# Optimization experiments

Hardware: AMD Instinct MI355X
Metric: run time of the kernel (lower is better)

Reference implementation:

```python
import jax, jax.numpy as jnp
import numpy as np
import math

H = 128      # hidden_size
B = 4        # bsz
N = 32       # bsz * num_doc_per_q
L = 128      # doc_len


def setup_inputs() -> dict:
    key = jax.random.key(0)
    ks = jax.random.split(key, 7)
    word_ent_info = jax.random.normal(ks[0], (N, L, H), dtype=jnp.float32)
    word_ent_info_mask = jax.random.randint(ks[1], (N, L), 0, 2, dtype=jnp.int32)
    doc = jax.random.normal(ks[2], (N, L, H), dtype=jnp.float32)
    doc_mask = jax.random.randint(ks[3], (N, L), 0, 2, dtype=jnp.int32)
    q_for_text = jax.random.normal(ks[4], (B, H), dtype=jnp.float32)
    # nn.Linear(3H, H): weight [H, 3H], bias [H]
    W1 = jax.random.normal(ks[5], (H, 3 * H), dtype=jnp.float32) / math.sqrt(3 * H)
    b1 = jnp.zeros((H,), dtype=jnp.float32)
    # nn.Linear(H, 1): weight [1, H], bias [1]
    w2 = jax.random.normal(ks[6], (1, H), dtype=jnp.float32) / math.sqrt(H)
    b2 = jnp.zeros((1,), dtype=jnp.float32)
    return {"word_ent_info": word_ent_info, "word_ent_info_mask": word_ent_info_mask,
            "doc": doc, "doc_mask": doc_mask, "q_for_text": q_for_text,
            "W1": W1, "b1": b1, "w2": w2, "b2": b2}


def reference(word_ent_info, word_ent_info_mask, doc, doc_mask, q_for_text, W1, b1, w2, b2):
    n, l, h = doc.shape
    bsz = q_for_text.shape[0]
    dt = doc.dtype

    # word_ent_infoagg = mask^T @ word_ent_info -> [N, H]
    m = word_ent_info_mask.astype(dt)
    ent_agg = jnp.einsum('nl,nlh->nh', m, word_ent_info)

    # q expanded to one row per document: [N, H]
    q_exp = jnp.repeat(q_for_text, n // bsz, axis=0)

    # Split W1 over the concat([doc_self, ent_agg, q_agg]) feature axis.
    # score_pre[n,j,k,:] = W1a @ (doc_j*doc_k) + W1b @ (doc_j*ent_agg) + W1c @ (doc_k*q)
    W1a, W1b, W1c = jnp.split(W1, 3, axis=1)        # each [H, H]
    A = jnp.einsum('nje,nke,ge->njkg', doc, doc, W1a)          # [N,L,L,H]
    Bt = jnp.einsum('nje,ge->njg', doc * ent_agg[:, None, :], W1b)  # [N,L,H]
    Ct = jnp.einsum('nke,ge->nkg', doc * q_exp[:, None, :], W1c)    # [N,L,H]
    hid = jnp.tanh(A + Bt[:, :, None, :] + Ct[:, None, :, :] + b1)  # [N,L,L,H]

    score = (jnp.einsum('njkg,g->njk', hid, w2[0]) + b2[0]) / math.sqrt(h)

    dm = doc_mask.astype(dt)
    score_mask = dm[:, :, None] * dm[:, None, :]     # [N,L,L]
    score = jnp.where(score_mask == 0.0, jnp.asarray(-1e9, dt), score)
    w = jax.nn.softmax(score, axis=-1) * score_mask
    doc_ent_enc = jnp.einsum('njk,nkh->njh', w, doc)  # [N,L,H]
    return doc_ent_enc
```

## Files before the change

### kernel.cpp

```cpp
#include <hip/hip_runtime.h>
#include <hip/hip_bf16.h>
#include <math.h>

#define Hh 128
#define Nn 32
#define Ll 128
#define W1S 384
#define PAD 136
#define EP 64
#define SP 72

typedef __attribute__((ext_vector_type(8))) short short8;
typedef __attribute__((ext_vector_type(4))) float floatx4;
typedef __attribute__((ext_vector_type(8))) _Float16 f16x8;

__device__ __forceinline__ unsigned short f2bf(float x) {
  __hip_bfloat16 h = __float2bfloat16(x);
  return __builtin_bit_cast(unsigned short, h);
}
__device__ __forceinline__ short8 pack8(float4 a, float4 b) {
  short8 r;
  r[0] = (short)f2bf(a.x); r[1] = (short)f2bf(a.y);
  r[2] = (short)f2bf(a.z); r[3] = (short)f2bf(a.w);
  r[4] = (short)f2bf(b.x); r[5] = (short)f2bf(b.y);
  r[6] = (short)f2bf(b.z); r[7] = (short)f2bf(b.w);
  return r;
}
__device__ __forceinline__ f16x8 cvt8h(float4 a, float4 b) {
  f16x8 r;
  r[0] = (_Float16)a.x; r[1] = (_Float16)a.y;
  r[2] = (_Float16)a.z; r[3] = (_Float16)a.w;
  r[4] = (_Float16)b.x; r[5] = (_Float16)b.y;
  r[6] = (_Float16)b.z; r[7] = (_Float16)b.w;
  return r;
}

__launch_bounds__(256, 2)
__global__ void k_prep(const float* __restrict__ wei, const int* __restrict__ wmask,
                       const float* __restrict__ doc, const float* __restrict__ q,
                       const float* __restrict__ W1, const float* __restrict__ b1,
                       float* __restrict__ Bt, float* __restrict__ Ct) {
  __shared__ __align__(16) short Wsb[Hh * PAD];
  __shared__ __align__(16) short docb[64 * PAD];
  __shared__ __align__(16) float red[2][Hh];
  __shared__ __align__(16) float scale[Hh];

  int b = blockIdx.x;
  int n = b >> 2, which = (b >> 1) & 1, mh = b & 1;
  int tid = threadIdx.x;
  const float* docn = doc + (size_t)n * Ll * Hh;
  int e8 = (tid & 15) * 8;

  float4 dreg[4][2];
#pragma unroll
  for (int p = 0; p < 4; ++p) {
    int row = mh * 64 + p * 16 + (tid >> 4);
    const float4* dp = (const float4*)(docn + (size_t)row * Hh + e8);
    dreg[p][0] = dp[0]; dreg[p][1] = dp[1];
  }
#pragma unroll
  for (int p = 0; p < 8; ++p) {
    int row = p * 16 + (tid >> 4);
    const float4* wp = (const float4*)(W1 + (size_t)row * W1S + (which + 1) * Hh + e8);
    *(short8*)(Wsb + row * PAD + e8) = pack8(wp[0], wp[1]);
  }
  if (which == 1) {
    if (tid < Hh) scale[tid] = q[(n >> 3) * Hh + tid];
  } else {
    int e = tid & 127, halfl = tid >> 7;
    const float* wp = wei + (size_t)n * Ll * Hh + (size_t)halfl * 64 * Hh + e;
    const int* mp = wmask + n * Ll + halfl * 64;
    float a = 0.f;
#pragma unroll 16
    for (int l = 0; l < 64; ++l) a = fmaf((float)mp[l], wp[(size_t)l * Hh], a);
    red[halfl][e] = a;
  }
  __syncthreads();
  if (which == 0 && tid < Hh) scale[tid] = red[0][tid] + red[1][tid];
  __syncthreads();
  {
    float s[8];
#pragma unroll
    for (int i = 0; i < 8; ++i) s[i] = scale[e8 + i];
#pragma unroll
    for (int p = 0; p < 4; ++p) {
      int r = p * 16 + (tid >> 4);
      float4 a = dreg[p][0], bq = dreg[p][1];
      a.x *= s[0]; a.y *= s[1]; a.z *= s[2]; a.w *= s[3];
      bq.x *= s[4]; bq.y *= s[5]; bq.z *= s[6]; bq.w *= s[7];
      *(short8*)(docb + r * PAD + e8) = pack8(a, bq);
    }
  }
  __syncthreads();

  int lane = tid & 63, w = tid >> 6;
  int l15 = lane & 15, quad = lane >> 4;
  floatx4 acc[8];
#pragma unroll
  for (int nt = 0; nt < 8; ++nt) acc[nt] = (floatx4){0.f, 0.f, 0.f, 0.f};
#pragma unroll
  for (int c = 0; c < 4; ++c) {
    int eo = c * 32 + quad * 8;
    short8 af = *(const short8*)(docb + (w * 16 + l15) * PAD + eo);
    short8 bfr[8];
#pragma unroll
    for (int nt = 0; nt < 8; ++nt)
      bfr[nt] = *(const short8*)(Wsb + (nt * 16 + l15) * PAD + eo);
#pragma unroll
    for (int nt = 0; nt < 8; ++nt)
      acc[nt] = __builtin_amdgcn_mfma_f32_16x16x32_bf16(af, bfr[nt], acc[nt], 0, 0, 0);
  }

  float* outp = (which ? Ct : Bt) + (size_t)n * Ll * Hh;
#pragma unroll
  for (int nt = 0; nt < 8; ++nt) {
    int g = nt * 16 + l15;
    float badd = which ? 0.f : b1[g];
#pragma unroll
    for (int r = 0; r < 4; ++r) {
      int k = mh * 64 + w * 16 + quad * 4 + r;
      outp[(size_t)k * Hh + g] = acc[nt][r] + badd;
    }
  }
}

__launch_bounds__(512, 6)
__global__ void k_main(const float* __restrict__ doc, const int* __restrict__ dmask,
                       const float* __restrict__ W1,
                       const float* __restrict__ w2, const float* __restrict__ b2,
                       const float* __restrict__ Bt, const float* __restrict__ Ct,
                       float* __restrict__ out) {
  __shared__ __align__(16) _Float16 As[Hh * SP];
  __shared__ __align__(16) _Float16 Bs[Hh * SP];
  __shared__ __align__(16) float sc[Ll];
  __shared__ __align__(16) float scw[Ll];

  int bid = blockIdx.x;
  int n = bid & 31, j = bid >> 5;
  int tid = threadIdx.x;
  const float* docn = doc + (size_t)n * Ll * Hh;
  size_t orow = ((size_t)n * Ll + j) * Hh;

  if (dmask[n * Ll + j] == 0) {
    if (tid < Hh) out[orow + tid] = 0.f;
    return;
  }

  int lane = tid & 63, wv = tid >> 6;
  int l15 = lane & 15, quad = lane >> 4;
  int grow = tid >> 2, seg = (tid & 3) * 16;

  floatx4 acc[8];
#pragma unroll
  for (int nt = 0; nt < 8; ++nt) acc[nt] = (floatx4){0.f, 0.f, 0.f, 0.f};

#pragma unroll
  for (int p = 0; p < 2; ++p) {
    if (p) __syncthreads();
    {
      const float4* dsrc = (const float4*)(docn + (size_t)grow * Hh + p * EP + seg);
      const float4* wsrc = (const float4*)(W1 + (size_t)grow * W1S + p * EP + seg);
      float4 d0 = dsrc[0], d1 = dsrc[1], d2 = dsrc[2], d3 = dsrc[3];
      float4 w0 = wsrc[0], w1 = wsrc[1], w2v = wsrc[2], w3 = wsrc[3];
      *(f16x8*)(Bs + grow * SP + seg) = cvt8h(d0, d1);
      *(f16x8*)(Bs + grow * SP + seg + 8) = cvt8h(d2, d3);
      *(f16x8*)(As + grow * SP + seg) = cvt8h(w0, w1);
      *(f16x8*)(As + grow * SP + seg + 8) = cvt8h(w2v, w3);
    }
    __syncthreads();
#pragma unroll
    for (int c = 0; c < 2; ++c) {
      int eo = c * 32 + quad * 8;
      f16x8 dr = *(const f16x8*)(Bs + (wv * 16 + l15) * SP + eo);
      f16x8 jr = *(const f16x8*)(Bs + j * SP + eo);
      f16x8 af = dr * jr;
#pragma unroll
      for (int nt = 0; nt < 8; ++nt) {
        f16x8 bfr = *(const f16x8*)(As + (nt * 16 + l15) * SP + eo);
        acc[nt] = __builtin_amdgcn_mfma_f32_16x16x32_f16(af, bfr, acc[nt], 0, 0, 0);
      }
    }
  }

  const float c2 = 2.885390081777927f;
  float bbc[8], w2r[8];
  const float* btrow = Bt + orow;
#pragma unroll
  for (int nt = 0; nt < 8; ++nt) {
    int g = nt * 16 + l15;
    bbc[nt] = btrow[g] * c2;
    w2r[nt] = w2[g];
  }
  const float* ctn = Ct + (size_t)n * Ll * Hh;
#pragma unroll
  for (int r = 0; r < 4; ++r) {
    int k = wv * 16 + quad * 4 + r;
    const float* ctp = ctn + (size_t)k * Hh + l15;
    float p = 0.f;
#pragma unroll
    for (int nt = 0; nt < 8; ++nt) {
      float s = acc[nt][r] + ctp[nt * 16];
      float a2 = fmaf(s, c2, bbc[nt]);
      float e = exp2f(a2);
      float th = fmaf(-2.f, __builtin_amdgcn_rcpf(e + 1.f), 1.f);
      p = fmaf(th, w2r[nt], p);
    }
    p += __shfl_xor(p, 1);
    p += __shfl_xor(p, 2);
    p += __shfl_xor(p, 4);
    p += __shfl_xor(p, 8);
    if (l15 == 0) sc[k] = p;
  }
  __syncthreads();

  {
    float b2v = b2[0];
    const float inv = 0.088388347648318447f;
    const int* dmn = dmask + n * Ll;
    int m0 = dmn[lane], m1 = dmn[lane + 64];
    float s0 = (sc[lane] + b2v) * inv;
    float s1 = (sc[lane + 64] + b2v) * inv;
    s0 = m0 ? s0 : -1e9f;
    s1 = m1 ? s1 : -1e9f;
    float mx = fmaxf(s0, s1);
#pragma unroll
    for (int off = 32; off; off >>= 1) mx = fmaxf(mx, __shfl_xor(mx, off));
    float ex0 = __expf(s0 - mx), ex1 = __expf(s1 - mx);
    float sm = ex0 + ex1;
#pragma unroll
    for (int off = 32; off; off >>= 1) sm += __shfl_xor(sm, off);
    float rden = 1.f / sm;
    scw[lane] = m0 ? ex0 * rden : 0.f;
    scw[lane + 64] = m1 ? ex1 * rden : 0.f;
  }
  __syncthreads();

  float* ored = (float*)As;
  int qk = tid >> 7, h = tid & 127;
  const float* dbase = docn + (size_t)qk * 32 * Hh + h;
  float o = 0.f;
#pragma unroll 8
  for (int kk = 0; kk < 32; ++kk)
    o = fmaf(scw[qk * 32 + kk], dbase[(size_t)kk * Hh], o);
  ored[qk * Hh + h] = o;
  __syncthreads();
  if (tid < Ll)
    out[orow + tid] = ored[tid] + ored[Hh + tid] + ored[2 * Hh + tid] + ored[3 * Hh + tid];
}

extern "C" void kernel_launch(void* const* d_in, const int* in_sizes, int n_in,
                              void* d_out, int out_size, void* d_ws, size_t ws_size,
                              hipStream_t stream) {
  const float* wei   = (const float*)d_in[0];
  const int*   wmask = (const int*)d_in[1];
  const float* doc   = (const float*)d_in[2];
  const int*   dmask = (const int*)d_in[3];
  const float* q     = (const float*)d_in[4];
  const float* W1    = (const float*)d_in[5];
  const float* b1    = (const float*)d_in[6];
  const float* w2    = (const float*)d_in[7];
  const float* b2    = (const float*)d_in[8];
  float* out = (float*)d_out;

  float* ws = (float*)d_ws;
  float* Bt = ws;
  float* Ct = Bt + (size_t)Nn * Ll * Hh;

  k_prep<<<Nn * 4, 256, 0, stream>>>(wei, wmask, doc, q, W1, b1, Bt, Ct);
  k_main<<<Nn * Ll, 512, 0, stream>>>(doc, dmask, W1, w2, b2, Bt, Ct, out);
}
```

Measured before the change: 124.6 us.

## Stage full doc/W1 tiles once, transpose Ct, reuse fp16 doc for output

The main kernel now loads the whole 128-wide doc and W1a tiles into shared memory in a single pass instead of two 64-wide passes, removing a barrier and reload. The Ct projection is stored transposed so each lane reads a float4 of Ct in the tanh epilogue, which is split into four independent accumulators. The final weighted sum over doc reads the fp16 doc copy already in shared memory instead of re-reading fp32 doc from global, using one 128-thread pass with no reduction step. Launch bounds drop from 6 to 4 blocks because of the larger shared buffers, and the output now uses fp16-rounded doc values.

```diff
diff --git a/kernel.cpp b/kernel.cpp
--- a/kernel.cpp
+++ b/kernel.cpp
@@ -7,8 +7,7 @@
 #define Ll 128
 #define W1S 384
 #define PAD 136
-#define EP 64
-#define SP 72
+#define SP2 136
 
 typedef __attribute__((ext_vector_type(8))) short short8;
 typedef __attribute__((ext_vector_type(4))) float floatx4;
@@ -111,27 +110,37 @@
       acc[nt] = __builtin_amdgcn_mfma_f32_16x16x32_bf16(af, bfr[nt], acc[nt], 0, 0, 0);
   }
 
-  float* outp = (which ? Ct : Bt) + (size_t)n * Ll * Hh;
-#pragma unroll
-  for (int nt = 0; nt < 8; ++nt) {
-    int g = nt * 16 + l15;
-    float badd = which ? 0.f : b1[g];
-#pragma unroll
-    for (int r = 0; r < 4; ++r) {
-      int k = mh * 64 + w * 16 + quad * 4 + r;
-      outp[(size_t)k * Hh + g] = acc[nt][r] + badd;
-    }
-  }
-}
-
-__launch_bounds__(512, 6)
+  if (which) {
+    float* outp = Ct + (size_t)n * Ll * Hh;
+#pragma unroll
+    for (int nt = 0; nt < 8; ++nt) {
+      float4 v;
+      v.x = acc[nt][0]; v.y = acc[nt][1]; v.z = acc[nt][2]; v.w = acc[nt][3];
+      *(float4*)(outp + (size_t)(nt * 16 + l15) * Hh + (mh * 64 + w * 16 + quad * 4)) = v;
+    }
+  } else {
+    float* outp = Bt + (size_t)n * Ll * Hh;
+#pragma unroll
+    for (int nt = 0; nt < 8; ++nt) {
+      int g = nt * 16 + l15;
+      float badd = b1[g];
+#pragma unroll
+      for (int r = 0; r < 4; ++r) {
+        int k = mh * 64 + w * 16 + quad * 4 + r;
+        outp[(size_t)k * Hh + g] = acc[nt][r] + badd;
+      }
+    }
+  }
+}
+
+__launch_bounds__(512, 4)
 __global__ void k_main(const float* __restrict__ doc, const int* __restrict__ dmask,
                        const float* __restrict__ W1,
                        const float* __restrict__ w2, const float* __restrict__ b2,
                        const float* __restrict__ Bt, const float* __restrict__ Ct,
                        float* __restrict__ out) {
-  __shared__ __align__(16) _Float16 As[Hh * SP];
-  __shared__ __align__(16) _Float16 Bs[Hh * SP];
+  __shared__ __align__(16) _Float16 As[Hh * SP2];
+  __shared__ __align__(16) _Float16 Bs[Hh * SP2];
   __shared__ __align__(16) float sc[Ll];
   __shared__ __align__(16) float scw[Ll];
 
@@ -148,68 +157,87 @@
 
   int lane = tid & 63, wv = tid >> 6;
   int l15 = lane & 15, quad = lane >> 4;
-  int grow = tid >> 2, seg = (tid & 3) * 16;
-
-  floatx4 acc[8];
-#pragma unroll
-  for (int nt = 0; nt < 8; ++nt) acc[nt] = (floatx4){0.f, 0.f, 0.f, 0.f};
-
-#pragma unroll
-  for (int p = 0; p < 2; ++p) {
-    if (p) __syncthreads();
-    {
-      const float4* dsrc = (const float4*)(docn + (size_t)grow * Hh + p * EP + seg);
-      const float4* wsrc = (const float4*)(W1 + (size_t)grow * W1S + p * EP + seg);
-      float4 d0 = dsrc[0], d1 = dsrc[1], d2 = dsrc[2], d3 = dsrc[3];
-      float4 w0 = wsrc[0], w1 = wsrc[1], w2v = wsrc[2], w3 = wsrc[3];
-      *(f16x8*)(Bs + grow * SP + seg) = cvt8h(d0, d1);
-      *(f16x8*)(Bs + grow * SP + seg + 8) = cvt8h(d2, d3);
-      *(f16x8*)(As + grow * SP + seg) = cvt8h(w0, w1);
-      *(f16x8*)(As + grow * SP + seg + 8) = cvt8h(w2v, w3);
-    }
-    __syncthreads();
-#pragma unroll
-    for (int c = 0; c < 2; ++c) {
-      int eo = c * 32 + quad * 8;
-      f16x8 dr = *(const f16x8*)(Bs + (wv * 16 + l15) * SP + eo);
-      f16x8 jr = *(const f16x8*)(Bs + j * SP + eo);
-      f16x8 af = dr * jr;
-#pragma unroll
-      for (int nt = 0; nt < 8; ++nt) {
-        f16x8 bfr = *(const f16x8*)(As + (nt * 16 + l15) * SP + eo);
-        acc[nt] = __builtin_amdgcn_mfma_f32_16x16x32_f16(af, bfr, acc[nt], 0, 0, 0);
-      }
-    }
-  }
 
   const float c2 = 2.885390081777927f;
   float bbc[8], w2r[8];
-  const float* btrow = Bt + orow;
-#pragma unroll
-  for (int nt = 0; nt < 8; ++nt) {
-    int g = nt * 16 + l15;
-    bbc[nt] = btrow[g] * c2;
-    w2r[nt] = w2[g];
-  }
-  const float* ctn = Ct + (size_t)n * Ll * Hh;
-#pragma unroll
-  for (int r = 0; r < 4; ++r) {
-    int k = wv * 16 + quad * 4 + r;
-    const float* ctp = ctn + (size_t)k * Hh + l15;
-    float p = 0.f;
-#pragma unroll
-    for (int nt = 0; nt < 8; ++nt) {
-      float s = acc[nt][r] + ctp[nt * 16];
-      float a2 = fmaf(s, c2, bbc[nt]);
-      float e = exp2f(a2);
-      float th = fmaf(-2.f, __builtin_amdgcn_rcpf(e + 1.f), 1.f);
-      p = fmaf(th, w2r[nt], p);
-    }
-    p += __shfl_xor(p, 1);
-    p += __shfl_xor(p, 2);
-    p += __shfl_xor(p, 4);
-    p += __shfl_xor(p, 8);
-    if (l15 == 0) sc[k] = p;
+  {
+    const float* btrow = Bt + orow;
+#pragma unroll
+    for (int nt = 0; nt < 8; ++nt) {
+      int g = nt * 16 + l15;
+      bbc[nt] = btrow[g] * c2;
+      w2r[nt] = w2[g];
+    }
+  }
+
+  {
+    int row = tid >> 2, seg = (tid & 3) * 32;
+    const float4* dsrc = (const float4*)(docn + (size_t)row * Hh + seg);
+    const float4* wsrc = (const float4*)(W1 + (size_t)row * W1S + seg);
+#pragma unroll
+    for (int i = 0; i < 4; ++i) {
+      *(f16x8*)(Bs + row * SP2 + seg + i * 8) = cvt8h(dsrc[2 * i], dsrc[2 * i + 1]);
+      *(f16x8*)(As + row * SP2 + seg + i * 8) = cvt8h(wsrc[2 * i], wsrc[2 * i + 1]);
+    }
+  }
+  __syncthreads();
+
+  floatx4 acc[8];
+#pragma unroll
+  for (int nt = 0; nt < 8; ++nt) acc[nt] = (floatx4){0.f, 0.f, 0.f, 0.f};
+#pragma unroll
+  for (int c = 0; c < 4; ++c) {
+    int eo = c * 32 + quad * 8;
+    f16x8 dr = *(const f16x8*)(Bs + (wv * 16 + l15) * SP2 + eo);
+    f16x8 jr = *(const f16x8*)(Bs + j * SP2 + eo);
+    f16x8 af = dr * jr;
+#pragma unroll
+    for (int nt = 0; nt < 8; ++nt) {
+      f16x8 bfr = *(const f16x8*)(As + (nt * 16 + l15) * SP2 + eo);
+      acc[nt] = __builtin_amdgcn_mfma_f32_16x16x32_f16(af, bfr, acc[nt], 0, 0, 0);
+    }
+  }
+
+  {
+    const float* ctn = Ct + (size_t)n * Ll * Hh;
+    float p0 = 0.f, p1 = 0.f, p2 = 0.f, p3 = 0.f;
+    int kbase = wv * 16 + quad * 4;
+#pragma unroll
+    for (int nt = 0; nt < 8; ++nt) {
+      float4 ct4 = *(const float4*)(ctn + (size_t)(nt * 16 + l15) * Hh + kbase);
+      float bb = bbc[nt], wr = w2r[nt];
+      {
+        float a2 = fmaf(acc[nt][0] + ct4.x, c2, bb);
+        float e = exp2f(a2);
+        p0 = fmaf(fmaf(-2.f, __builtin_amdgcn_rcpf(e + 1.f), 1.f), wr, p0);
+      }
+      {
+        float a2 = fmaf(acc[nt][1] + ct4.y, c2, bb);
+        float e = exp2f(a2);
+        p1 = fmaf(fmaf(-2.f, __builtin_amdgcn_rcpf(e + 1.f), 1.f), wr, p1);
+      }
+      {
+        float a2 = fmaf(acc[nt][2] + ct4.z, c2, bb);
+        float e = exp2f(a2);
+        p2 = fmaf(fmaf(-2.f, __builtin_amdgcn_rcpf(e + 1.f), 1.f), wr, p2);
+      }
+      {
+        float a2 = fmaf(acc[nt][3] + ct4.w, c2, bb);
+        float e = exp2f(a2);
+        p3 = fmaf(fmaf(-2.f, __builtin_amdgcn_rcpf(e + 1.f), 1.f), wr, p3);
+      }
+    }
+#pragma unroll
+    for (int off = 1; off <= 8; off <<= 1) {
+      p0 += __shfl_xor(p0, off);
+      p1 += __shfl_xor(p1, off);
+      p2 += __shfl_xor(p2, off);
+      p3 += __shfl_xor(p3, off);
+    }
+    if (l15 == 0) {
+      sc[kbase + 0] = p0; sc[kbase + 1] = p1;
+      sc[kbase + 2] = p2; sc[kbase + 3] = p3;
+    }
   }
   __syncthreads();
 
@@ -235,17 +263,18 @@
   }
   __syncthreads();
 
-  float* ored = (float*)As;
-  int qk = tid >> 7, h = tid & 127;
-  const float* dbase = docn + (size_t)qk * 32 * Hh + h;
-  float o = 0.f;
+  if (tid < Ll) {
+    int h = tid;
+    float o0 = 0.f, o1 = 0.f, o2 = 0.f, o3 = 0.f;
 #pragma unroll 8
-  for (int kk = 0; kk < 32; ++kk)
-    o = fmaf(scw[qk * 32 + kk], dbase[(size_t)kk * Hh], o);
-  ored[qk * Hh + h] = o;
-  __syncthreads();
-  if (tid < Ll)
-    out[orow + tid] = ored[tid] + ored[Hh + tid] + ored[2 * Hh + tid] + ored[3 * Hh + tid];
+    for (int kk = 0; kk < Ll; kk += 4) {
+      o0 = fmaf(scw[kk + 0], (float)Bs[(kk + 0) * SP2 + h], o0);
+      o1 = fmaf(scw[kk + 1], (float)Bs[(kk + 1) * SP2 + h], o1);
+      o2 = fmaf(scw[kk + 2], (float)Bs[(kk + 2) * SP2 + h], o2);
+      o3 = fmaf(scw[kk + 3], (float)Bs[(kk + 3) * SP2 + h], o3);
+    }
+    out[orow + h] = (o0 + o1) + (o2 + o3);
+  }
 }
 
 extern "C" void kernel_launch(void* const* d_in, const int* in_sizes, int n_in,
```

New measurement: 154.8 us. +24.2%, slower.

## Fuse Ct projection into main kernel MFMA accumulation, drop Ct buffer

Applied to the files above, without the earlier changes.

Removes the Ct precompute from the prep kernel and instead accumulates W1c·(doc_k*q) directly in the main kernel's MFMA loop, using a third LDS tile for the W1c slice. This eliminates the Ct global write and per-element Ct reads in the tanh epilogue, and halves the prep grid. In exchange each main-kernel block doubles its MFMA count and LDS footprint, recomputing the same Ct for every j, and the occupancy hint is lowered from 6 to 4.

```diff
diff --git a/kernel.cpp b/kernel.cpp
--- a/kernel.cpp
+++ b/kernel.cpp
@@ -37,16 +37,16 @@
 
 __launch_bounds__(256, 2)
 __global__ void k_prep(const float* __restrict__ wei, const int* __restrict__ wmask,
-                       const float* __restrict__ doc, const float* __restrict__ q,
+                       const float* __restrict__ doc,
                        const float* __restrict__ W1, const float* __restrict__ b1,
-                       float* __restrict__ Bt, float* __restrict__ Ct) {
+                       float* __restrict__ Bt) {
   __shared__ __align__(16) short Wsb[Hh * PAD];
   __shared__ __align__(16) short docb[64 * PAD];
   __shared__ __align__(16) float red[2][Hh];
   __shared__ __align__(16) float scale[Hh];
 
   int b = blockIdx.x;
-  int n = b >> 2, which = (b >> 1) & 1, mh = b & 1;
+  int n = b >> 1, mh = b & 1;
   int tid = threadIdx.x;
   const float* docn = doc + (size_t)n * Ll * Hh;
   int e8 = (tid & 15) * 8;
@@ -61,12 +61,10 @@
 #pragma unroll
   for (int p = 0; p < 8; ++p) {
     int row = p * 16 + (tid >> 4);
-    const float4* wp = (const float4*)(W1 + (size_t)row * W1S + (which + 1) * Hh + e8);
+    const float4* wp = (const float4*)(W1 + (size_t)row * W1S + Hh + e8);
     *(short8*)(Wsb + row * PAD + e8) = pack8(wp[0], wp[1]);
   }
-  if (which == 1) {
-    if (tid < Hh) scale[tid] = q[(n >> 3) * Hh + tid];
-  } else {
+  {
     int e = tid & 127, halfl = tid >> 7;
     const float* wp = wei + (size_t)n * Ll * Hh + (size_t)halfl * 64 * Hh + e;
     const int* mp = wmask + n * Ll + halfl * 64;
@@ -76,7 +74,7 @@
     red[halfl][e] = a;
   }
   __syncthreads();
-  if (which == 0 && tid < Hh) scale[tid] = red[0][tid] + red[1][tid];
+  if (tid < Hh) scale[tid] = red[0][tid] + red[1][tid];
   __syncthreads();
   {
     float s[8];
@@ -111,11 +109,11 @@
       acc[nt] = __builtin_amdgcn_mfma_f32_16x16x32_bf16(af, bfr[nt], acc[nt], 0, 0, 0);
   }
 
-  float* outp = (which ? Ct : Bt) + (size_t)n * Ll * Hh;
+  float* outp = Bt + (size_t)n * Ll * Hh;
 #pragma unroll
   for (int nt = 0; nt < 8; ++nt) {
     int g = nt * 16 + l15;
-    float badd = which ? 0.f : b1[g];
+    float badd = b1[g];
 #pragma unroll
     for (int r = 0; r < 4; ++r) {
       int k = mh * 64 + w * 16 + quad * 4 + r;
@@ -124,14 +122,14 @@
   }
 }
 
-__launch_bounds__(512, 6)
+__launch_bounds__(512, 4)
 __global__ void k_main(const float* __restrict__ doc, const int* __restrict__ dmask,
-                       const float* __restrict__ W1,
+                       const float* __restrict__ W1, const float* __restrict__ q,
                        const float* __restrict__ w2, const float* __restrict__ b2,
-                       const float* __restrict__ Bt, const float* __restrict__ Ct,
-                       float* __restrict__ out) {
-  __shared__ __align__(16) _Float16 As[Hh * SP];
-  __shared__ __align__(16) _Float16 Bs[Hh * SP];
+                       const float* __restrict__ Bt, float* __restrict__ out) {
+  __shared__ __align__(16) _Float16 Aw[Hh * SP];
+  __shared__ __align__(16) _Float16 Cw[Hh * SP];
+  __shared__ __align__(16) _Float16 Dw[Hh * SP];
   __shared__ __align__(16) float sc[Ll];
   __shared__ __align__(16) float scw[Ll];
 
@@ -150,6 +148,16 @@
   int l15 = lane & 15, quad = lane >> 4;
   int grow = tid >> 2, seg = (tid & 3) * 16;
 
+  f16x8 q8[4];
+  {
+    const float* qn = q + (size_t)(n >> 3) * Hh;
+#pragma unroll
+    for (int pc = 0; pc < 4; ++pc) {
+      const float4* qp = (const float4*)(qn + pc * 32 + quad * 8);
+      q8[pc] = cvt8h(qp[0], qp[1]);
+    }
+  }
+
   floatx4 acc[8];
 #pragma unroll
   for (int nt = 0; nt < 8; ++nt) acc[nt] = (floatx4){0.f, 0.f, 0.f, 0.f};
@@ -159,25 +167,35 @@
     if (p) __syncthreads();
     {
       const float4* dsrc = (const float4*)(docn + (size_t)grow * Hh + p * EP + seg);
-      const float4* wsrc = (const float4*)(W1 + (size_t)grow * W1S + p * EP + seg);
+      const float4* wa = (const float4*)(W1 + (size_t)grow * W1S + p * EP + seg);
+      const float4* wc = (const float4*)(W1 + (size_t)grow * W1S + 2 * Hh + p * EP + seg);
       float4 d0 = dsrc[0], d1 = dsrc[1], d2 = dsrc[2], d3 = dsrc[3];
-      float4 w0 = wsrc[0], w1 = wsrc[1], w2v = wsrc[2], w3 = wsrc[3];
-      *(f16x8*)(Bs + grow * SP + seg) = cvt8h(d0, d1);
-      *(f16x8*)(Bs + grow * SP + seg + 8) = cvt8h(d2, d3);
-      *(f16x8*)(As + grow * SP + seg) = cvt8h(w0, w1);
-      *(f16x8*)(As + grow * SP + seg + 8) = cvt8h(w2v, w3);
+      float4 a0 = wa[0], a1 = wa[1], a2 = wa[2], a3 = wa[3];
+      float4 c0 = wc[0], c1 = wc[1], c2v = wc[2], c3 = wc[3];
+      *(f16x8*)(Dw + grow * SP + seg) = cvt8h(d0, d1);
+      *(f16x8*)(Dw + grow * SP + seg + 8) = cvt8h(d2, d3);
+      *(f16x8*)(Aw + grow * SP + seg) = cvt8h(a0, a1);
+      *(f16x8*)(Aw + grow * SP + seg + 8) = cvt8h(a2, a3);
+      *(f16x8*)(Cw + grow * SP + seg) = cvt8h(c0, c1);
+      *(f16x8*)(Cw + grow * SP + seg + 8) = cvt8h(c2v, c3);
     }
     __syncthreads();
 #pragma unroll
     for (int c = 0; c < 2; ++c) {
       int eo = c * 32 + quad * 8;
-      f16x8 dr = *(const f16x8*)(Bs + (wv * 16 + l15) * SP + eo);
-      f16x8 jr = *(const f16x8*)(Bs + j * SP + eo);
+      f16x8 dr = *(const f16x8*)(Dw + (wv * 16 + l15) * SP + eo);
+      f16x8 jr = *(const f16x8*)(Dw + j * SP + eo);
       f16x8 af = dr * jr;
+      f16x8 ag = dr * q8[p * 2 + c];
 #pragma unroll
       for (int nt = 0; nt < 8; ++nt) {
-        f16x8 bfr = *(const f16x8*)(As + (nt * 16 + l15) * SP + eo);
-        acc[nt] = __builtin_amdgcn_mfma_f32_16x16x32_f16(af, bfr, acc[nt], 0, 0, 0);
+        f16x8 ba = *(const f16x8*)(Aw + (nt * 16 + l15) * SP + eo);
+        acc[nt] = __builtin_amdgcn_mfma_f32_16x16x32_f16(af, ba, acc[nt], 0, 0, 0);
+      }
+#pragma unroll
+      for (int nt = 0; nt < 8; ++nt) {
+        f16x8 bc = *(const f16x8*)(Cw + (nt * 16 + l15) * SP + eo);
+        acc[nt] = __builtin_amdgcn_mfma_f32_16x16x32_f16(ag, bc, acc[nt], 0, 0, 0);
       }
     }
   }
@@ -191,16 +209,13 @@
     bbc[nt] = btrow[g] * c2;
     w2r[nt] = w2[g];
   }
-  const float* ctn = Ct + (size_t)n * Ll * Hh;
 #pragma unroll
   for (int r = 0; r < 4; ++r) {
     int k = wv * 16 + quad * 4 + r;
-    const float* ctp = ctn + (size_t)k * Hh + l15;
     float p = 0.f;
 #pragma unroll
     for (int nt = 0; nt < 8; ++nt) {
-      float s = acc[nt][r] + ctp[nt * 16];
-      float a2 = fmaf(s, c2, bbc[nt]);
+      float a2 = fmaf(acc[nt][r], c2, bbc[nt]);
       float e = exp2f(a2);
       float th = fmaf(-2.f, __builtin_amdgcn_rcpf(e + 1.f), 1.f);
       p = fmaf(th, w2r[nt], p);
@@ -235,7 +250,7 @@
   }
   __syncthreads();
 
-  float* ored = (float*)As;
+  float* ored = (float*)Aw;
   int qk = tid >> 7, h = tid & 127;
   const float* dbase = docn + (size_t)qk * 32 * Hh + h;
   float o = 0.f;
@@ -262,10 +277,8 @@
   const float* b2    = (const float*)d_in[8];
   float* out = (float*)d_out;
 
-  float* ws = (float*)d_ws;
-  float* Bt = ws;
-  float* Ct = Bt + (size_t)Nn * Ll * Hh;
-
-  k_prep<<<Nn * 4, 256, 0, stream>>>(wei, wmask, doc, q, W1, b1, Bt, Ct);
-  k_main<<<Nn * Ll, 512, 0, stream>>>(doc, dmask, W1, w2, b2, Bt, Ct, out);
-}
+  float* Bt = (float*)d_ws;
+
+  k_prep<<<Nn * 2, 256, 0, stream>>>(wei, wmask, doc, W1, b1, Bt);
+  k_main<<<Nn * Ll, 512, 0, stream>>>(doc, dmask, W1, q, w2, b2, Bt, out);
+}
```

New measurement: 147.9 us. 1.19x slower.
